# Performance work log

Hardware: AMD Instinct MI355X
Metric: run time of the kernel (lower is better)

Reference implementation:

```python
import jax, jax.numpy as jnp
import numpy as np

M, D_H, D_K, D_V = 8, 512, 64, 64
B, N = 16, 1024

def _xavier(key, shape, gain=1.414):
    fan_in, fan_out = shape[-2], shape[-1]
    limit = gain * (6.0 / (fan_in + fan_out)) ** 0.5
    return jax.random.uniform(key, shape, jnp.float32, -limit, limit)

def setup_inputs() -> dict:
    key = jax.random.key(0)
    kH, kq, kk, kv, ko = jax.random.split(key, 5)
    return {
        "H": jax.random.normal(kH, (B, N, D_H), jnp.float32),
        "W_Q": _xavier(kq, (M, D_H, D_K)),
        "W_K": _xavier(kk, (M, D_H, D_K)),
        "W_V": _xavier(kv, (M, D_H, D_V)),
        "W_O": _xavier(ko, (M, D_V, D_H)),
    }

def reference(H, W_Q, W_K, W_V, W_O):
    # H: [B, n, d_h]; per-head projections -> [B, M, n, d_k/d_v]
    Q = jnp.einsum('bnd,mdq->bmnq', H, W_Q)
    K = jnp.einsum('bnd,mdk->bmnk', H, W_K)
    V = jnp.einsum('bnd,mdv->bmnv', H, W_V)
    scale = 1.0 / jnp.sqrt(jnp.float32(W_K.shape[-1]))
    U = scale * jnp.einsum('bmnq,bmkq->bmnk', Q, K)  # [B, M, n, n]
    A = jax.nn.softmax(U, axis=-1)
    Hp = jnp.einsum('bmnk,bmkv->bmnv', A, V)          # [B, M, n, d_v]
    # per-head output projection then sum over heads (dim=-3)
    return jnp.einsum('bmnv,mvd->bnd', Hp, W_O)       # [B, n, d_h]
```

## Files before the change

kernel.cpp:

```cpp
#include <hip/hip_runtime.h>
#include <hip/hip_bf16.h>

typedef __attribute__((ext_vector_type(8))) short bf16x8;
typedef __attribute__((ext_vector_type(4))) float f32x4;
typedef __attribute__((ext_vector_type(16))) float f32x16;
typedef __attribute__((ext_vector_type(2))) unsigned uint2v;

__device__ __forceinline__ ushort f2bf(float f) {
  union { float f; unsigned u; } v; v.f = f;
  unsigned r = v.u + 0x7FFFu + ((v.u >> 16) & 1u);
  return (ushort)(r >> 16);
}

__device__ __forceinline__ float exp2_(float x) {
#if __has_builtin(__builtin_amdgcn_exp2f)
  return __builtin_amdgcn_exp2f(x);
#else
  return exp2f(x);
#endif
}

__device__ __forceinline__ unsigned cvtpk(float lo, float hi) {
  unsigned r;
  asm("v_cvt_pk_bf16_f32 %0, %1, %2" : "=v"(r) : "v"(lo), "v"(hi));
  return r;
}

__device__ __forceinline__ uint2v lane32_swap(unsigned a, unsigned b) {
#if __has_builtin(__builtin_amdgcn_permlane32_swap)
  return __builtin_amdgcn_permlane32_swap(a, b, false, false);
#else
  unsigned sa = (unsigned)__shfl_xor((int)a, 32);
  unsigned sb = (unsigned)__shfl_xor((int)b, 32);
  bool lo = ((threadIdx.x & 32) == 0);
  uint2v r;
  r.x = lo ? a : sb;
  r.y = lo ? sa : b;
  return r;
#endif
}

__device__ __forceinline__ void gload_lds16(const ushort* g, ushort* l) {
  __builtin_amdgcn_global_load_lds(
      (const __attribute__((address_space(1))) void*)g,
      (__attribute__((address_space(3))) void*)l, 16, 0, 0);
}

template <int N>
__device__ __forceinline__ void vmw() {
  asm volatile("s_waitcnt vmcnt(%0)" ::"i"(N) : "memory");
}

#define QSCALE 0.18033688011112042f

__global__ void __launch_bounds__(256) prep_kernel(
    const float* __restrict__ H, const float* __restrict__ WQ,
    const float* __restrict__ WK, const float* __restrict__ WV,
    const float* __restrict__ WO, ushort* __restrict__ Hb,
    ushort* __restrict__ Wqkv, ushort* __restrict__ Wo) {
  int bid = blockIdx.x;
  if (bid < 4096) {
    int i = (bid * 256 + threadIdx.x) * 8;
    float4 a = *(const float4*)(H + i);
    float4 b = *(const float4*)(H + i + 4);
    uint4 o;
    o.x = f2bf(a.x) | ((unsigned)f2bf(a.y) << 16);
    o.y = f2bf(a.z) | ((unsigned)f2bf(a.w) << 16);
    o.z = f2bf(b.x) | ((unsigned)f2bf(b.y) << 16);
    o.w = f2bf(b.z) | ((unsigned)f2bf(b.w) << 16);
    *(uint4*)(Hb + i) = o;
  } else if (bid < 7168) {
    int t = (bid - 4096) * 256 + threadIdx.x;
    int j = t >> 9, d = t & 511;
    int m = j / 192, r = j % 192, which = r >> 6, dk = r & 63;
    const float* W = (which == 0) ? WQ : (which == 1) ? WK : WV;
    Wqkv[t] = f2bf(W[(m * 512 + d) * 64 + dk]);
  } else {
    int t = (bid - 7168) * 256 + threadIdx.x;
    int j = t >> 9, mv = t & 511;
    Wo[t] = f2bf(WO[mv * 512 + j]);
  }
}

template <int EPI>
__global__ void __launch_bounds__(256, 2) gemm_bt_pipe(
    const ushort* __restrict__ A, const ushort* __restrict__ Bt,
    float* __restrict__ C, int Kdim, int Ncols,
    ushort* __restrict__ Qo, ushort* __restrict__ Ko, ushort* __restrict__ Vo) {
  __shared__ __align__(16) ushort S[32768];
  ushort* SA = S;
  ushort* SB = S + 16384;

  const int tid = threadIdx.x, lane = tid & 63, w = tid >> 6;
  const int hi = lane >> 4, l15 = lane & 15, l3 = lane & 3;
  const int wm = w >> 1, wn = w & 1;

  const int gx = gridDim.x;
  const int nwg = gx * gridDim.y;
  const int bid = blockIdx.y * gx + blockIdx.x;
  const int id2 = (bid & 7) * (nwg >> 3) + (bid >> 3);
  const int brow = (id2 / gx) * 128, bcol = (id2 % gx) * 128;

  const int srow = w * 32 + (lane >> 2);
  const int sslot = ((lane & 3) ^ ((lane >> 2) & 3)) * 8;
  const ushort* aS = A + (size_t)(brow + srow) * Kdim + sslot;
  const ushort* bS = Bt + (size_t)(bcol + srow) * Kdim + sslot;

  f32x4 acc[4][4];
  const f32x4 z4 = {0.f, 0.f, 0.f, 0.f};
#pragma unroll
  for (int i = 0; i < 4; ++i)
#pragma unroll
    for (int j = 0; j < 4; ++j) acc[i][j] = z4;

  auto STAGE = [&](int T, int h, int buf) {
    const ushort* a0 = aS + T * 64 + h * 32;
    const ushort* b0 = bS + T * 64 + h * 32;
    ushort* la = SA + buf * 8192 + h * 4096 + (w * 32) * 32;
    ushort* lb = SB + buf * 8192 + h * 4096 + (w * 32) * 32;
    gload_lds16(a0, la);
    gload_lds16(a0 + (size_t)16 * Kdim, la + 512);
    gload_lds16(b0, lb);
    gload_lds16(b0 + (size_t)16 * Kdim, lb + 512);
  };

  auto LOADF = [&](int buf, int h, bf16x8* af, bf16x8* bf) {
    const ushort* Ab = SA + buf * 8192 + h * 4096;
    const ushort* Bb = SB + buf * 8192 + h * 4096;
#pragma unroll
    for (int fr = 0; fr < 4; ++fr) {
      int r = wm * 64 + fr * 16 + l15;
      af[fr] = *(const bf16x8*)&Ab[r * 32 + ((hi ^ l3) << 3)];
    }
#pragma unroll
    for (int fc = 0; fc < 4; ++fc) {
      int r = wn * 64 + fc * 16 + l15;
      bf[fc] = *(const bf16x8*)&Bb[r * 32 + ((hi ^ l3) << 3)];
    }
  };

  auto MFMA16 = [&](bf16x8* af, bf16x8* bf) {
#pragma unroll
    for (int i = 0; i < 4; ++i)
#pragma unroll
      for (int j = 0; j < 4; ++j)
        acc[i][j] = __builtin_amdgcn_mfma_f32_16x16x32_bf16(af[i], bf[j], acc[i][j], 0, 0, 0);
  };

  STAGE(0, 0, 0);
  STAGE(0, 1, 0);
  STAGE(1, 0, 1);
  vmw<8>();
  __builtin_amdgcn_s_barrier();

#pragma unroll
  for (int t = 0; t < 8; ++t) {
    const int buf = t & 1;
    {
      bf16x8 af[4], bf[4];
      LOADF(buf, 0, af, bf);
      if (t < 7) STAGE(t + 1, 1, buf ^ 1);
      if (t < 7) vmw<8>(); else vmw<0>();
      __builtin_amdgcn_s_barrier();
      asm volatile("s_waitcnt lgkmcnt(0)" ::: "memory");
      __builtin_amdgcn_sched_barrier(0);
      __builtin_amdgcn_s_setprio(1);
      MFMA16(af, bf);
      __builtin_amdgcn_s_setprio(0);
      __builtin_amdgcn_s_barrier();
    }
    {
      bf16x8 af[4], bf[4];
      LOADF(buf, 1, af, bf);
      if (t < 6) STAGE(t + 2, 0, buf);
      if (t < 6) vmw<8>(); else if (t == 6) vmw<4>(); else vmw<0>();
      __builtin_amdgcn_s_barrier();
      asm volatile("s_waitcnt lgkmcnt(0)" ::: "memory");
      __builtin_amdgcn_sched_barrier(0);
      __builtin_amdgcn_s_setprio(1);
      MFMA16(af, bf);
      __builtin_amdgcn_s_setprio(0);
      __builtin_amdgcn_s_barrier();
    }
  }

#pragma unroll
  for (int i = 0; i < 4; ++i) {
    int row0 = brow + wm * 64 + i * 16 + hi * 4;
#pragma unroll
    for (int j = 0; j < 4; ++j) {
      int col = bcol + wn * 64 + j * 16 + l15;
      if (EPI == 0) {
#pragma unroll
        for (int q = 0; q < 4; ++q)
          C[(size_t)(row0 + q) * Ncols + col] = acc[i][j][q];
      } else {
        int m = col / 192, r = col % 192, which = r >> 6, dk = r & 63;
        ushort* base = (which == 0) ? Qo : (which == 1) ? Ko : Vo;
        float cs = (which == 0) ? QSCALE : 1.0f;
#pragma unroll
        for (int q = 0; q < 4; ++q) {
          int row = row0 + q;
          int bb = row >> 10, n = row & 1023;
          base[(size_t)((bb * 8 + m) * 1024 + n) * 64 + dk] = f2bf(acc[i][j][q] * cs);
        }
      }
    }
  }
}

__global__ void __launch_bounds__(256) transpose_v_kernel(const ushort* __restrict__ V,
                                                          ushort* __restrict__ Vt) {
  __shared__ __align__(16) ushort T[64][72];
  int bm = blockIdx.x >> 4, nt = blockIdx.x & 15;
  const ushort* src = V + (size_t)bm * 65536 + nt * 64 * 64;
  int tid = threadIdx.x;
#pragma unroll
  for (int i = 0; i < 2; ++i) {
    int c = tid + i * 256;
    int row = c >> 3, cc = (c & 7) * 8;
    *(uint4*)&T[row][cc] = *(const uint4*)(src + c * 8);
  }
  __syncthreads();
  int v = tid >> 2, nn0 = (tid & 3) * 16;
  ushort tmp[16];
#pragma unroll
  for (int k = 0; k < 16; ++k) tmp[k] = T[nn0 + k][v];
  ushort* dst = Vt + (size_t)bm * 65536 + v * 1024 + nt * 64 + nn0;
  *(uint4*)(dst + 0) = *(uint4*)&tmp[0];
  *(uint4*)(dst + 8) = *(uint4*)&tmp[8];
}

__global__ void __launch_bounds__(256, 2) attn_kernel(const ushort* __restrict__ Q,
                                                      const ushort* __restrict__ K,
                                                      const ushort* __restrict__ Vt,
                                                      ushort* __restrict__ Hp) {
  __shared__ __align__(16) ushort Ks[2][64 * 64];
  __shared__ __align__(16) ushort Vs[2][64 * 64];

  int wk = (blockIdx.x & 7) * 64 + (blockIdx.x >> 3);
  const int bm = wk >> 2, qt = wk & 3;
  const int b = bm >> 3, m = bm & 7;
  const int tid = threadIdx.x, lane = tid & 63, w = tid >> 6;
  const int hi = lane >> 5, l31 = lane & 31;
  const ushort* Qp = Q + (size_t)bm * 65536;
  const ushort* Kp = K + (size_t)bm * 65536;
  const ushort* Vp = Vt + (size_t)bm * 65536;
  const int qw = qt * 256 + w * 64;

  bf16x8 qb[2][4];
#pragma unroll
  for (int qs = 0; qs < 2; ++qs)
#pragma unroll
    for (int s = 0; s < 4; ++s)
      qb[qs][s] = *(const bf16x8*)(Qp + (size_t)(qw + qs * 32 + l31) * 64 + s * 16 + hi * 8);

  bf16x8 ones;
#pragma unroll
  for (int j = 0; j < 8; ++j) ones[j] = (short)0x3F80;

  f32x16 oacc[2][2], lacc[2];
#pragma unroll
  for (int r = 0; r < 16; ++r) {
    oacc[0][0][r] = 0.f; oacc[0][1][r] = 0.f;
    oacc[1][0][r] = 0.f; oacc[1][1][r] = 0.f;
    lacc[0][r] = 0.f; lacc[1][r] = 0.f;
  }

  const int sr = tid >> 2, sc4 = (tid & 3) << 4;
  const unsigned bo0 = ((unsigned)(sc4 * 2)) ^ (((unsigned)(sr & 7)) << 4);

  {
    uint4 k0 = *(const uint4*)(Kp + (size_t)sr * 64 + sc4);
    uint4 k1 = *(const uint4*)(Kp + (size_t)sr * 64 + sc4 + 8);
    uint4 v0 = *(const uint4*)(Vp + (size_t)sr * 1024 + sc4);
    uint4 v1 = *(const uint4*)(Vp + (size_t)sr * 1024 + sc4 + 8);
    char* kd = (char*)&Ks[0][sr * 64];
    char* vd = (char*)&Vs[0][sr * 64];
    *(uint4*)(kd + bo0) = k0; *(uint4*)(kd + (bo0 ^ 16)) = k1;
    *(uint4*)(vd + bo0) = v0; *(uint4*)(vd + (bo0 ^ 16)) = v1;
  }
  __syncthreads();

  int cur = 0;
  for (int kt = 0; kt < 16; ++kt) {
    uint4 k0, k1, v0, v1;
    const bool pf = (kt < 15);
    if (pf) {
      int n0 = (kt + 1) * 64;
      k0 = *(const uint4*)(Kp + (size_t)(n0 + sr) * 64 + sc4);
      k1 = *(const uint4*)(Kp + (size_t)(n0 + sr) * 64 + sc4 + 8);
      v0 = *(const uint4*)(Vp + (size_t)sr * 1024 + n0 + sc4);
      v1 = *(const uint4*)(Vp + (size_t)sr * 1024 + n0 + sc4 + 8);
    }

    const ushort* kbase = &Ks[cur][0];
    bf16x8 kA[2][4];
#pragma unroll
    for (int ja = 0; ja < 2; ++ja) {
      int row = ja * 32 + l31;
      const char* kr = (const char*)(kbase + row * 64);
#pragma unroll
      for (int s = 0; s < 4; ++s)
        kA[ja][s] = *(const bf16x8*)(kr + (((unsigned)(s * 32 + hi * 16)) ^ (((unsigned)(row & 7)) << 4)));
    }

    f32x16 st[2][2];
#pragma unroll
    for (int qs = 0; qs < 2; ++qs)
#pragma unroll
      for (int ja = 0; ja < 2; ++ja) {
#pragma unroll
        for (int r = 0; r < 16; ++r) st[qs][ja][r] = 0.f;
#pragma unroll
        for (int s = 0; s < 4; ++s)
          st[qs][ja] = __builtin_amdgcn_mfma_f32_32x32x16_bf16(kA[ja][s], qb[qs][s], st[qs][ja], 0, 0, 0);
      }

    bf16x8 pb[2][4];
#pragma unroll
    for (int qs = 0; qs < 2; ++qs) {
#pragma unroll
      for (int r = 0; r < 16; ++r) {
        st[qs][0][r] = exp2_(st[qs][0][r]);
        st[qs][1][r] = exp2_(st[qs][1][r]);
      }

#pragma unroll
      for (int ja = 0; ja < 2; ++ja) {
#pragma unroll
        for (int g = 0; g < 2; ++g) {
          unsigned x0 = cvtpk(st[qs][ja][g * 8 + 0], st[qs][ja][g * 8 + 1]);
          unsigned x1 = cvtpk(st[qs][ja][g * 8 + 2], st[qs][ja][g * 8 + 3]);
          unsigned y0 = cvtpk(st[qs][ja][g * 8 + 4], st[qs][ja][g * 8 + 5]);
          unsigned y1 = cvtpk(st[qs][ja][g * 8 + 6], st[qs][ja][g * 8 + 7]);
          uint2v s0 = lane32_swap(x0, y0);
          uint2v s1 = lane32_swap(x1, y1);
          uint4 wv; wv.x = s0.x; wv.y = s1.x; wv.z = s0.y; wv.w = s1.y;
          pb[qs][ja * 2 + g] = *(bf16x8*)&wv;
        }
      }

#pragma unroll
      for (int ks = 0; ks < 4; ++ks)
        lacc[qs] = __builtin_amdgcn_mfma_f32_32x32x16_bf16(ones, pb[qs][ks], lacc[qs], 0, 0, 0);
    }

    const ushort* vbase = &Vs[cur][0];
#pragma unroll
    for (int vj = 0; vj < 2; ++vj) {
      int row = vj * 32 + l31;
      const char* vr = (const char*)(vbase + row * 64);
      bf16x8 va[4];
#pragma unroll
      for (int ks = 0; ks < 4; ++ks)
        va[ks] = *(const bf16x8*)(vr + (((unsigned)(ks * 32 + hi * 16)) ^ (((unsigned)(row & 7)) << 4)));
#pragma unroll
      for (int qs = 0; qs < 2; ++qs)
#pragma unroll
        for (int ks = 0; ks < 4; ++ks)
          oacc[qs][vj] = __builtin_amdgcn_mfma_f32_32x32x16_bf16(va[ks], pb[qs][ks], oacc[qs][vj], 0, 0, 0);
    }

    if (pf) {
      char* kd = (char*)&Ks[cur ^ 1][sr * 64];
      char* vd = (char*)&Vs[cur ^ 1][sr * 64];
      *(uint4*)(kd + bo0) = k0; *(uint4*)(kd + (bo0 ^ 16)) = k1;
      *(uint4*)(vd + bo0) = v0; *(uint4*)(vd + (bo0 ^ 16)) = v1;
    }
    __syncthreads();
    cur ^= 1;
  }

#pragma unroll
  for (int qs = 0; qs < 2; ++qs) {
    float linv = 1.0f / lacc[qs][0];
    int q = qw + qs * 32 + l31;
    size_t ro = ((size_t)b * 1024 + q) * 512 + m * 64;
#pragma unroll
    for (int vj = 0; vj < 2; ++vj)
#pragma unroll
      for (int t4 = 0; t4 < 4; ++t4) {
        ushort4 o;
        o.x = f2bf(oacc[qs][vj][t4 * 4 + 0] * linv);
        o.y = f2bf(oacc[qs][vj][t4 * 4 + 1] * linv);
        o.z = f2bf(oacc[qs][vj][t4 * 4 + 2] * linv);
        o.w = f2bf(oacc[qs][vj][t4 * 4 + 3] * linv);
        *(ushort4*)(Hp + ro + vj * 32 + t4 * 8 + hi * 4) = o;
      }
  }
}

extern "C" void kernel_launch(void* const* d_in, const int* in_sizes, int n_in,
                              void* d_out, int out_size, void* d_ws, size_t ws_size,
                              hipStream_t stream) {
  const float* H  = (const float*)d_in[0];
  const float* WQ = (const float*)d_in[1];
  const float* WK = (const float*)d_in[2];
  const float* WV = (const float*)d_in[3];
  const float* WO = (const float*)d_in[4];
  float* out = (float*)d_out;

  ushort* ws   = (ushort*)d_ws;
  ushort* Hb   = ws;
  ushort* Wqkv = Hb + 16384 * 512;
  ushort* Wo   = Wqkv + 1536 * 512;
  ushort* Qb   = Wo + 512 * 512;
  ushort* Kb   = Qb + 128 * 1024 * 64;
  ushort* Vb   = Kb + 128 * 1024 * 64;
  ushort* Vtb  = Vb + 128 * 1024 * 64;
  ushort* Hp   = Vtb + 128 * 1024 * 64;

  prep_kernel<<<8192, 256, 0, stream>>>(H, WQ, WK, WV, WO, Hb, Wqkv, Wo);
  gemm_bt_pipe<1><<<dim3(12, 128), 256, 0, stream>>>(Hb, Wqkv, nullptr, 512, 1536,
                                                     Qb, Kb, Vb);
  transpose_v_kernel<<<2048, 256, 0, stream>>>(Vb, Vtb);
  attn_kernel<<<512, 256, 0, stream>>>(Qb, Kb, Vtb, Hp);
  gemm_bt_pipe<0><<<dim3(4, 128), 256, 0, stream>>>(Hp, Wo, out, 512, 512,
                                                    nullptr, nullptr, nullptr);
}
```

Before: 117.0 us.

## Restructure projection GEMM pipeline to full 64-wide K tiles with 8-way swizzle

The projection GEMM now stages each full 64-element K tile per buffer with an 8-slot XOR swizzle, where it previously used two 32-wide halves with a 4-slot swizzle. Each iteration loads all fragments for both halves, issues the next global-to-LDS prefetch right after the barrier, and runs 32 MFMAs per sync point. This roughly halves the barriers and waits per K step and overlaps the prefetch with the MFMA block. In exchange each wave holds more fragment registers, and a single barrier now guards the buffer reuse.

Result: faster. 114.7 us (median of 2 runs) (-2.0%).

```diff
diff --git a/kernel.cpp b/kernel.cpp
--- a/kernel.cpp
+++ b/kernel.cpp
@@ -92,7 +92,7 @@
   ushort* SB = S + 16384;
 
   const int tid = threadIdx.x, lane = tid & 63, w = tid >> 6;
-  const int hi = lane >> 4, l15 = lane & 15, l3 = lane & 3;
+  const int hs = lane >> 4, l15 = lane & 15;
   const int wm = w >> 1, wn = w & 1;
 
   const int gx = gridDim.x;
@@ -101,8 +101,8 @@
   const int id2 = (bid & 7) * (nwg >> 3) + (bid >> 3);
   const int brow = (id2 / gx) * 128, bcol = (id2 % gx) * 128;
 
-  const int srow = w * 32 + (lane >> 2);
-  const int sslot = ((lane & 3) ^ ((lane >> 2) & 3)) * 8;
+  const int srow = w * 32 + (lane >> 3);
+  const int sslot = ((lane & 7) ^ (lane >> 3)) * 8;
   const ushort* aS = A + (size_t)(brow + srow) * Kdim + sslot;
   const ushort* bS = Bt + (size_t)(bcol + srow) * Kdim + sslot;
 
@@ -113,80 +113,66 @@
 #pragma unroll
     for (int j = 0; j < 4; ++j) acc[i][j] = z4;
 
-  auto STAGE = [&](int T, int h, int buf) {
-    const ushort* a0 = aS + T * 64 + h * 32;
-    const ushort* b0 = bS + T * 64 + h * 32;
-    ushort* la = SA + buf * 8192 + h * 4096 + (w * 32) * 32;
-    ushort* lb = SB + buf * 8192 + h * 4096 + (w * 32) * 32;
-    gload_lds16(a0, la);
-    gload_lds16(a0 + (size_t)16 * Kdim, la + 512);
-    gload_lds16(b0, lb);
-    gload_lds16(b0 + (size_t)16 * Kdim, lb + 512);
+  auto STAGE = [&](int T, int buf) {
+    ushort* la = SA + buf * 8192 + (w * 32) * 64;
+    ushort* lb = SB + buf * 8192 + (w * 32) * 64;
+#pragma unroll
+    for (int g = 0; g < 4; ++g) {
+      gload_lds16(aS + T * 64 + (size_t)(g * 8) * Kdim, la + g * 8 * 64);
+      gload_lds16(bS + T * 64 + (size_t)(g * 8) * Kdim, lb + g * 8 * 64);
+    }
   };
 
-  auto LOADF = [&](int buf, int h, bf16x8* af, bf16x8* bf) {
-    const ushort* Ab = SA + buf * 8192 + h * 4096;
-    const ushort* Bb = SB + buf * 8192 + h * 4096;
-#pragma unroll
-    for (int fr = 0; fr < 4; ++fr) {
-      int r = wm * 64 + fr * 16 + l15;
-      af[fr] = *(const bf16x8*)&Ab[r * 32 + ((hi ^ l3) << 3)];
-    }
-#pragma unroll
-    for (int fc = 0; fc < 4; ++fc) {
-      int r = wn * 64 + fc * 16 + l15;
-      bf[fc] = *(const bf16x8*)&Bb[r * 32 + ((hi ^ l3) << 3)];
+  auto LOADF = [&](int buf, bf16x8 af[2][4], bf16x8 bf[2][4]) {
+    const ushort* Ab = SA + buf * 8192;
+    const ushort* Bb = SB + buf * 8192;
+#pragma unroll
+    for (int h = 0; h < 2; ++h) {
+#pragma unroll
+      for (int fr = 0; fr < 4; ++fr) {
+        int r = wm * 64 + fr * 16 + l15;
+        int c = (h * 4 + hs) ^ (r & 7);
+        af[h][fr] = *(const bf16x8*)&Ab[r * 64 + c * 8];
+      }
+#pragma unroll
+      for (int fc = 0; fc < 4; ++fc) {
+        int r = wn * 64 + fc * 16 + l15;
+        int c = (h * 4 + hs) ^ (r & 7);
+        bf[h][fc] = *(const bf16x8*)&Bb[r * 64 + c * 8];
+      }
     }
   };
 
-  auto MFMA16 = [&](bf16x8* af, bf16x8* bf) {
-#pragma unroll
-    for (int i = 0; i < 4; ++i)
-#pragma unroll
-      for (int j = 0; j < 4; ++j)
-        acc[i][j] = __builtin_amdgcn_mfma_f32_16x16x32_bf16(af[i], bf[j], acc[i][j], 0, 0, 0);
-  };
-
-  STAGE(0, 0, 0);
-  STAGE(0, 1, 0);
-  STAGE(1, 0, 1);
+  STAGE(0, 0);
+  STAGE(1, 1);
   vmw<8>();
   __builtin_amdgcn_s_barrier();
 
 #pragma unroll
   for (int t = 0; t < 8; ++t) {
     const int buf = t & 1;
-    {
-      bf16x8 af[4], bf[4];
-      LOADF(buf, 0, af, bf);
-      if (t < 7) STAGE(t + 1, 1, buf ^ 1);
-      if (t < 7) vmw<8>(); else vmw<0>();
-      __builtin_amdgcn_s_barrier();
-      asm volatile("s_waitcnt lgkmcnt(0)" ::: "memory");
-      __builtin_amdgcn_sched_barrier(0);
-      __builtin_amdgcn_s_setprio(1);
-      MFMA16(af, bf);
-      __builtin_amdgcn_s_setprio(0);
-      __builtin_amdgcn_s_barrier();
-    }
-    {
-      bf16x8 af[4], bf[4];
-      LOADF(buf, 1, af, bf);
-      if (t < 6) STAGE(t + 2, 0, buf);
-      if (t < 6) vmw<8>(); else if (t == 6) vmw<4>(); else vmw<0>();
-      __builtin_amdgcn_s_barrier();
-      asm volatile("s_waitcnt lgkmcnt(0)" ::: "memory");
-      __builtin_amdgcn_sched_barrier(0);
-      __builtin_amdgcn_s_setprio(1);
-      MFMA16(af, bf);
-      __builtin_amdgcn_s_setprio(0);
-      __builtin_amdgcn_s_barrier();
-    }
+    bf16x8 af[2][4], bf[2][4];
+    LOADF(buf, af, bf);
+    asm volatile("s_waitcnt lgkmcnt(0)" ::: "memory");
+    __builtin_amdgcn_sched_barrier(0);
+    __builtin_amdgcn_s_barrier();
+    if (t < 6) STAGE(t + 2, buf);
+    __builtin_amdgcn_s_setprio(1);
+#pragma unroll
+    for (int h = 0; h < 2; ++h)
+#pragma unroll
+      for (int i = 0; i < 4; ++i)
+#pragma unroll
+        for (int j = 0; j < 4; ++j)
+          acc[i][j] = __builtin_amdgcn_mfma_f32_16x16x32_bf16(af[h][i], bf[h][j], acc[i][j], 0, 0, 0);
+    __builtin_amdgcn_s_setprio(0);
+    if (t < 6) vmw<8>(); else if (t == 6) vmw<0>();
+    __builtin_amdgcn_s_barrier();
   }
 
 #pragma unroll
   for (int i = 0; i < 4; ++i) {
-    int row0 = brow + wm * 64 + i * 16 + hi * 4;
+    int row0 = brow + wm * 64 + i * 16 + hs * 4;
 #pragma unroll
     for (int j = 0; j < 4; ++j) {
       int col = bcol + wn * 64 + j * 16 + l15;
```
